# Performance work log

Hardware: AMD Instinct MI355X
Metric: run time of the kernel (lower is better)

Reference implementation:

```python
import jax, jax.numpy as jnp
import numpy as np

DIM, HEADS, MLP_RATIO = 384, 6, 4.0
HEAD_DIM = DIM // HEADS
HID = int(DIM * MLP_RATIO)
EPS = 1e-5


def _layer_norm(x, g, b):
    m = jnp.mean(x, axis=-1, keepdims=True)
    v = jnp.mean(jnp.square(x - m), axis=-1, keepdims=True)
    return (x - m) * jax.lax.rsqrt(v + EPS) * g + b


def setup_inputs() -> dict:
    key = jax.random.key(0)
    ks = jax.random.split(key, 16)
    B, N, C = 4, 2048, DIM
    s = 0.02
    return {
        "x": jax.random.normal(ks[0], (B, N, C), dtype=jnp.float32),
        "ln1_g": jnp.ones((C,), jnp.float32),
        "ln1_b": jnp.zeros((C,), jnp.float32),
        "qkv_w": jax.random.normal(ks[1], (C, 3 * C), jnp.float32) * s,  # [in, out]
        "qkv_b": jnp.zeros((3 * C,), jnp.float32),
        "proj_w": jax.random.normal(ks[2], (C, C), jnp.float32) * s,
        "proj_b": jnp.zeros((C,), jnp.float32),
        "ln2_g": jnp.ones((C,), jnp.float32),
        "ln2_b": jnp.zeros((C,), jnp.float32),
        "fc1_w": jax.random.normal(ks[3], (C, HID), jnp.float32) * s,
        "fc1_b": jnp.zeros((HID,), jnp.float32),
        "fc2_w": jax.random.normal(ks[4], (HID, C), jnp.float32) * s,
        "fc2_b": jnp.zeros((C,), jnp.float32),
    }


def reference(x, ln1_g, ln1_b, qkv_w, qkv_b, proj_w, proj_b,
              ln2_g, ln2_b, fc1_w, fc1_b, fc2_w, fc2_b):
    B, N, C = x.shape
    scale = HEAD_DIM ** (-0.5)

    # --- attention branch (pre-norm) ---
    h = _layer_norm(x, ln1_g, ln1_b)
    qkv = (h @ qkv_w + qkv_b).reshape(B, N, 3, HEADS, HEAD_DIM)
    qkv = jnp.transpose(qkv, (2, 0, 3, 1, 4))  # [3, B, H, N, D]
    q, k, v = qkv[0], qkv[1], qkv[2]
    attn = jnp.einsum("bhnd,bhmd->bhnm", q, k) * scale
    attn = jax.nn.softmax(attn, axis=-1)
    out = jnp.einsum("bhnm,bhmd->bhnd", attn, v)
    out = jnp.transpose(out, (0, 2, 1, 3)).reshape(B, N, C)
    x = x + (out @ proj_w + proj_b)

    # --- MLP branch (pre-norm) ---
    h = _layer_norm(x, ln2_g, ln2_b)
    h = jax.nn.gelu(h @ fc1_w + fc1_b, approximate=False)
    x = x + (h @ fc2_w + fc2_b)
    return x
```

## Files before the change

kernel.cpp:

```cpp
#include <hip/hip_runtime.h>

typedef unsigned short u16;
typedef unsigned int u32;
typedef __bf16 bf16x8_t __attribute__((ext_vector_type(8)));
typedef float f32x4 __attribute__((ext_vector_type(4)));
typedef float f32x16 __attribute__((ext_vector_type(16)));

__device__ __forceinline__ u16 f2b(float f) {
  union { float f; u32 u; } v; v.f = f;
  u32 r = v.u + 0x7fffu + ((v.u >> 16) & 1u);
  return (u16)(r >> 16);
}

__device__ __forceinline__ u32 pkbf(float a, float b) {
  union { __bf16 h[2]; u32 u; } v;
  v.h[0] = (__bf16)a; v.h[1] = (__bf16)b;
  return v.u;
}

__device__ __forceinline__ size_t fmoff(int r, int c, int Kd) {
  return ((size_t)(r >> 4) * (Kd >> 3) + (c >> 3)) * 128 + (r & 15) * 8 + (c & 7);
}

__device__ __forceinline__ f32x4 mfma16(uint4 a, uint4 b, f32x4 c) {
  return __builtin_amdgcn_mfma_f32_16x16x32_bf16(
      __builtin_bit_cast(bf16x8_t, a), __builtin_bit_cast(bf16x8_t, b), c, 0, 0, 0);
}

__device__ __forceinline__ f32x16 mfma32(uint4 a, uint4 b, f32x16 c) {
  return __builtin_amdgcn_mfma_f32_32x32x16_bf16(
      __builtin_bit_cast(bf16x8_t, a), __builtin_bit_cast(bf16x8_t, b), c, 0, 0, 0);
}

__device__ __forceinline__ void plswap(u32& a, u32& b) {
  asm("v_permlane32_swap_b32 %0, %1" : "+v"(a), "+v"(b));
}

__device__ __forceinline__ void load_lds16(const void* g, void* l) {
  __builtin_amdgcn_global_load_lds(
      (const __attribute__((address_space(1))) unsigned int*)g,
      (__attribute__((address_space(3))) unsigned int*)l, 16, 0, 0);
}

template <int N>
__device__ __forceinline__ void waitvm() {
  if constexpr (N == 0) asm volatile("s_waitcnt vmcnt(0)" ::: "memory");
  else if constexpr (N == 4) asm volatile("s_waitcnt vmcnt(4)" ::: "memory");
  else if constexpr (N == 6) asm volatile("s_waitcnt vmcnt(6)" ::: "memory");
  else if constexpr (N == 8) asm volatile("s_waitcnt vmcnt(8)" ::: "memory");
  else asm volatile("s_waitcnt vmcnt(10)" ::: "memory");
}

__device__ __forceinline__ void ln_body(const float* __restrict__ x,
                                        const float* __restrict__ g,
                                        const float* __restrict__ bta,
                                        u16* __restrict__ out, int row,
                                        int lane) {
  const float* xr = x + (size_t)row * 384;
  float v[6];
  float s = 0.f;
#pragma unroll
  for (int i = 0; i < 6; i++) { v[i] = xr[i * 64 + lane]; s += v[i]; }
#pragma unroll
  for (int off = 32; off >= 1; off >>= 1) s += __shfl_xor(s, off);
  float mean = s * (1.0f / 384.0f);
  float vs = 0.f;
#pragma unroll
  for (int i = 0; i < 6; i++) { float d = v[i] - mean; vs += d * d; }
#pragma unroll
  for (int off = 32; off >= 1; off >>= 1) vs += __shfl_xor(vs, off);
  float rstd = rsqrtf(vs * (1.0f / 384.0f) + 1e-5f);
#pragma unroll
  for (int i = 0; i < 6; i++) {
    int c = i * 64 + lane;
    out[fmoff(row, c, 384)] = f2b((v[i] - mean) * rstd * g[c] + bta[c]);
  }
}

__global__ __launch_bounds__(256) void ln_k(const float* __restrict__ x,
                                            const float* __restrict__ g,
                                            const float* __restrict__ bta,
                                            u16* __restrict__ out) {
  ln_body(x, g, bta, out, blockIdx.x * 4 + (threadIdx.x >> 6),
          threadIdx.x & 63);
}

__global__ __launch_bounds__(256) void prep_k(
    const float* __restrict__ w0, u16* __restrict__ t0_,
    const float* __restrict__ w1, u16* __restrict__ t1_,
    const float* __restrict__ w2, u16* __restrict__ t2_,
    const float* __restrict__ w3, u16* __restrict__ t3_,
    const float* __restrict__ x, const float* __restrict__ g,
    const float* __restrict__ bta, u16* __restrict__ lnout) {
  __shared__ u16 L[64][68];
  int tile = blockIdx.x, tid = threadIdx.x;
  if (tile >= 432) {
    ln_body(x, g, bta, lnout, (tile - 432) * 4 + (tid >> 6), tid & 63);
    return;
  }
  const float* w; u16* wt; int K, N, rel;
  if (tile < 108)      { w = w0; wt = t0_; K = 384;  N = 1152; rel = tile; }
  else if (tile < 144) { w = w1; wt = t1_; K = 384;  N = 384;  rel = tile - 108; }
  else if (tile < 288) { w = w2; wt = t2_; K = 384;  N = 1536; rel = tile - 144; }
  else                 { w = w3; wt = t3_; K = 1536; N = 384;  rel = tile - 288; }
  int ntx = N >> 6;
  int tk = (rel / ntx) << 6, tn = (rel - (rel / ntx) * ntx) << 6;

  int r = tid >> 2, c0 = (tid & 3) << 4;
  const float* src = w + (size_t)(tk + r) * N + tn + c0;
#pragma unroll
  for (int j = 0; j < 16; j += 4) {
    float4 a = *(const float4*)(src + j);
    L[r][c0 + j + 0] = f2b(a.x);
    L[r][c0 + j + 1] = f2b(a.y);
    L[r][c0 + j + 2] = f2b(a.z);
    L[r][c0 + j + 3] = f2b(a.w);
  }
  __syncthreads();
  int n = tid >> 2, k0 = (tid & 3) << 4;
  u16 tmp[16];
#pragma unroll
  for (int j = 0; j < 16; j++) tmp[j] = L[k0 + j][n];
  u16* dst = wt + (size_t)(tn + n) * K + tk + k0;
  *(uint4*)dst = *(const uint4*)(tmp);
  *(uint4*)(dst + 8) = *(const uint4*)(tmp + 8);
}

template <int EPI, int MR, int KD>
__global__ __launch_bounds__(256, 2) void gemm_k(
    const u16* __restrict__ A, const u16* __restrict__ Bt,
    const float* __restrict__ bias, const float* __restrict__ res,
    void* __restrict__ outp, int Nn,
    u16* __restrict__ qp, u16* __restrict__ kp, u16* __restrict__ vtp) {
  constexpr int NS = KD / 64;
  constexpr int KD8 = KD / 8;
  __shared__ __align__(16) u16 Bs[3][64 * 64];
  int tid = threadIdx.x;
  int lane = tid & 63, wid = tid >> 6;
  int li = lane & 15, lg = lane >> 4;
  int wr = wid >> 1, wc = wid & 1;
  int row0 = blockIdx.y * (MR * 32), col0 = blockIdx.x * 64;

  int lr = lane >> 3;
  int sc8 = ((lane & 7) ^ lr) * 8;

  const u16* Ab = A + ((size_t)(row0 / 16 + wr * MR) * KD8 + lg) * 128 + li * 8;

  f32x4 z = {0.f, 0.f, 0.f, 0.f};
  f32x4 acc[MR][2];
#pragma unroll
  for (int m = 0; m < MR; m++)
#pragma unroll
    for (int n = 0; n < 2; n++) acc[m][n] = z;

  uint4 af0[MR][2], af1[MR][2];

  auto stageB = [&](int buf, int k0) {
#pragma unroll
    for (int j = 0; j < 2; j++) {
      int ib = wid * 2 + j;
      load_lds16(Bt + (size_t)(col0 + ib * 8 + lr) * KD + k0 + sc8,
                 (char*)Bs[buf] + ib * 1024);
    }
  };
  auto loadA = [&](uint4 (*dst)[2], int t) {
#pragma unroll
    for (int m = 0; m < MR; m++)
#pragma unroll
      for (int kk = 0; kk < 2; kk++)
        dst[m][kk] =
            *(const uint4*)(Ab + ((size_t)m * KD8 + t * 8 + kk * 4) * 128);
  };

  stageB(0, 0);
  stageB(1, 64);
  loadA(af0, 0);
  if (NS > 1) loadA(af1, 1);
  waitvm<2 * MR>();
  __builtin_amdgcn_s_barrier();
  asm volatile("" ::: "memory");

#pragma unroll
  for (int t = 0; t < NS; t++) {
    if (t + 2 < NS) stageB((t + 2) % 3, (t + 2) * 64);
    const char* Bsb = (const char*)Bs[t % 3];
#pragma unroll
    for (int kk = 0; kk < 2; kk++) {
      uint4 bf[2];
#pragma unroll
      for (int n = 0; n < 2; n++) {
        int c = wc * 32 + n * 16 + li;
        bf[n] = *(const uint4*)(Bsb + c * 128 +
                                ((kk * 64 + lg * 16) ^ ((c & 7) << 4)));
      }
#pragma unroll
      for (int m = 0; m < MR; m++)
#pragma unroll
        for (int n = 0; n < 2; n++)
          acc[m][n] = mfma16((t & 1) ? af1[m][kk] : af0[m][kk], bf[n],
                             acc[m][n]);
    }
    if (t + 2 < NS) {
      if (t & 1) loadA(af1, t + 2);
      else       loadA(af0, t + 2);
      waitvm<2 + 2 * MR>();
      __builtin_amdgcn_s_barrier();
      asm volatile("" ::: "memory");
    } else if (t + 1 < NS) {
      waitvm<0>();
      __builtin_amdgcn_s_barrier();
      asm volatile("" ::: "memory");
    }
  }

#pragma unroll
  for (int m = 0; m < MR; m++) {
#pragma unroll
    for (int n = 0; n < 2; n++) {
#pragma unroll
      for (int j = 0; j < 4; j++) {
        int r = row0 + wr * (MR * 16) + m * 16 + lg * 4 + j;
        int c = col0 + wc * 32 + n * 16 + li;
        float v = acc[m][n][j] + bias[c];
        if (EPI == 0) {
          ((float*)outp)[(size_t)r * Nn + c] = v + res[(size_t)r * Nn + c];
        } else if (EPI == 1) {
          float e = __expf(-1.5957691f * v * (1.f + 0.044715f * v * v));
          ((u16*)outp)[fmoff(r, c, Nn)] = f2b(v / (1.f + e));
        } else {
          int tt = c / 384;
          int c2 = c - tt * 384;
          int hh = c2 >> 6, d = c2 & 63;
          int bb = r >> 11, nn = r & 2047;
          size_t bh = (size_t)bb * 6 + hh;
          int tile = nn >> 5;
          if (tt == 2) {
            int kvl = nn & 31;
            int kvHalf = (kvl >> 4) & 1, h2 = (kvl >> 3) & 1, jj = kvl & 7;
            int dTile = d >> 5, l31 = d & 31;
            vtp[(((bh * 64 + tile) * 2 + dTile) * 2 + kvHalf) * 512 +
                (l31 + h2 * 32) * 8 + jj] = f2b(v);
          } else {
            int chunk = d >> 4, h2 = (d >> 3) & 1, e = d & 7;
            int l31 = nn & 31;
            size_t off = ((bh * 64 + tile) * 4 + chunk) * 512 +
                         (l31 + h2 * 32) * 8 + e;
            if (tt == 0) qp[off] = f2b(v * 0.18033688f);
            else         kp[off] = f2b(v);
          }
        }
      }
    }
  }
}

__global__ __launch_bounds__(256, 3) void attn_k(const u16* __restrict__ q,
                                                 const u16* __restrict__ k,
                                                 const u16* __restrict__ vt,
                                                 u16* __restrict__ out) {
  __shared__ __align__(16) float Ol[3][2][16][64];
  __shared__ float Ls[3][64];

  int tid = threadIdx.x;
  int lane = tid & 63, wid = tid >> 6;
  int l31 = lane & 31, hi = lane >> 5;
  int bid = blockIdx.x;
  int nid = (bid & 7) * 192 + (bid >> 3);
  int bh = nid >> 6, qT = nid & 63;
  int b = bh / 6, hh = bh - b * 6;
  int qb = qT * 32;

  const u16* qp_ = q + ((size_t)bh * 64 + qT) * 2048 + lane * 8;
  const u16* kp_ = k + ((size_t)bh * 64 + wid * 16) * 2048 + lane * 8;
  const u16* vp_ = vt + ((size_t)bh * 64 + wid * 16) * 2048 + lane * 8;

  uint4 qf[4], kf[4];
#pragma unroll
  for (int c = 0; c < 4; c++) qf[c] = *(const uint4*)(qp_ + c * 512);
#pragma unroll
  for (int c = 0; c < 4; c++) kf[c] = *(const uint4*)(kp_ + c * 512);
  kp_ += 2048;

  f32x16 o0, o1;
#pragma unroll
  for (int r = 0; r < 16; r++) { o0[r] = 0.f; o1[r] = 0.f; }
  float lsum = 0.f;

#pragma unroll
  for (int t = 0; t < 16; t++) {
    uint4 vf0 = *(const uint4*)(vp_);
    uint4 vf1 = *(const uint4*)(vp_ + 512);
    uint4 vf2 = *(const uint4*)(vp_ + 1024);
    uint4 vf3 = *(const uint4*)(vp_ + 1536);
    uint4 kn[4];
    if (t < 15) {
#pragma unroll
      for (int c = 0; c < 4; c++) kn[c] = *(const uint4*)(kp_ + c * 512);
    }

    f32x16 s;
#pragma unroll
    for (int r = 0; r < 16; r++) s[r] = 0.f;
#pragma unroll
    for (int c = 0; c < 4; c++) s = mfma32(kf[c], qf[c], s);

    float p[16];
#pragma unroll
    for (int r = 0; r < 16; r++) p[r] = __builtin_amdgcn_exp2f(s[r]);
    lsum += ((p[0] + p[1]) + (p[2] + p[3])) + ((p[4] + p[5]) + (p[6] + p[7])) +
            ((p[8] + p[9]) + (p[10] + p[11])) +
            ((p[12] + p[13]) + (p[14] + p[15]));

    u32 u[8];
#pragma unroll
    for (int i = 0; i < 8; i++) u[i] = pkbf(p[2 * i], p[2 * i + 1]);
    plswap(u[0], u[2]); plswap(u[1], u[3]);
    plswap(u[4], u[6]); plswap(u[5], u[7]);
    uint4 pa0 = {u[0], u[1], u[2], u[3]};
    uint4 pa1 = {u[4], u[5], u[6], u[7]};

    o0 = mfma32(pa0, vf0, o0);
    o0 = mfma32(pa1, vf1, o0);
    o1 = mfma32(pa0, vf2, o1);
    o1 = mfma32(pa1, vf3, o1);

    if (t < 15) {
#pragma unroll
      for (int c = 0; c < 4; c++) kf[c] = kn[c];
    }
    kp_ += 2048;
    vp_ += 2048;
  }

  lsum += __shfl_xor(lsum, 32);

  if (wid) {
#pragma unroll
    for (int r = 0; r < 16; r++) {
      Ol[wid - 1][0][r][lane] = o0[r];
      Ol[wid - 1][1][r][lane] = o1[r];
    }
    Ls[wid - 1][lane] = lsum;
  }
  __syncthreads();
  if (wid == 0) {
#pragma unroll
    for (int w = 0; w < 3; w++) lsum += Ls[w][lane];
#pragma unroll
    for (int r = 0; r < 16; r++)
#pragma unroll
      for (int w = 0; w < 3; w++) {
        o0[r] += Ol[w][0][r][lane];
        o1[r] += Ol[w][1][r][lane];
      }
    float rl = 1.0f / lsum;
#pragma unroll
    for (int r = 0; r < 16; r++) {
      int qo = (r & 3) + 8 * (r >> 2) + hi * 4;
      float rlq = __shfl(rl, qo, 64);
      int row = b * 2048 + qb + qo;
      out[fmoff(row, hh * 64 + l31, 384)] = f2b(o0[r] * rlq);
      out[fmoff(row, hh * 64 + 32 + l31, 384)] = f2b(o1[r] * rlq);
    }
  }
}

extern "C" void kernel_launch(void* const* d_in, const int* in_sizes, int n_in,
                              void* d_out, int out_size, void* d_ws,
                              size_t ws_size, hipStream_t stream) {
  const float* x      = (const float*)d_in[0];
  const float* ln1_g  = (const float*)d_in[1];
  const float* ln1_b  = (const float*)d_in[2];
  const float* qkv_w  = (const float*)d_in[3];
  const float* qkv_b  = (const float*)d_in[4];
  const float* proj_w = (const float*)d_in[5];
  const float* proj_b = (const float*)d_in[6];
  const float* ln2_g  = (const float*)d_in[7];
  const float* ln2_b  = (const float*)d_in[8];
  const float* fc1_w  = (const float*)d_in[9];
  const float* fc1_b  = (const float*)d_in[10];
  const float* fc2_w  = (const float*)d_in[11];
  const float* fc2_b  = (const float*)d_in[12];
  float* out = (float*)d_out;

  char* p = (char*)d_ws;
  u16* qkvwt  = (u16*)p;  p += (size_t)1152 * 384 * 2;
  u16* projwt = (u16*)p;  p += (size_t)384 * 384 * 2;
  u16* fc1wt  = (u16*)p;  p += (size_t)1536 * 384 * 2;
  u16* fc2wt  = (u16*)p;  p += (size_t)384 * 1536 * 2;
  float* x1   = (float*)p; p += (size_t)8192 * 384 * 4;
  u16* reg1   = (u16*)p;  p += (size_t)8192 * 384 * 2;
  u16* reg2   = (u16*)p;  p += (size_t)8192 * 1536 * 2;
  u16* qd  = reg2;
  u16* kd  = reg2 + (size_t)24 * 2048 * 64;
  u16* vtd = kd + (size_t)24 * 2048 * 64;
  u16* h3  = reg2;

  prep_k<<<432 + 2048, 256, 0, stream>>>(qkv_w, qkvwt, proj_w, projwt,
                                         fc1_w, fc1wt, fc2_w, fc2wt,
                                         x, ln1_g, ln1_b, reg1);
  gemm_k<2, 4, 384><<<dim3(18, 64), 256, 0, stream>>>(
      reg1, qkvwt, qkv_b, nullptr, nullptr, 1152, qd, kd, vtd);
  attn_k<<<dim3(1536), 256, 0, stream>>>(qd, kd, vtd, reg1);
  gemm_k<0, 2, 384><<<dim3(6, 128), 256, 0, stream>>>(
      reg1, projwt, proj_b, x, x1, 384, nullptr, nullptr, nullptr);
  ln_k<<<2048, 256, 0, stream>>>(x1, ln2_g, ln2_b, reg1);
  gemm_k<1, 4, 384><<<dim3(24, 64), 256, 0, stream>>>(
      reg1, fc1wt, fc1_b, nullptr, h3, 1536, nullptr, nullptr, nullptr);
  gemm_k<0, 2, 1536><<<dim3(6, 128), 256, 0, stream>>>(
      h3, fc2wt, fc2_b, x1, out, 384, nullptr, nullptr, nullptr);
}
```

Measured before the change: 135.7 us.

## Swizzle GEMM block order, prefetch V in attention, split reduction across waves

GEMM launches become 1D grids with a swizzle that groups 8 row tiles per column tile for L2 reuse, and MR=2 GEMMs get a higher occupancy launch bound. In attention, V fragments are prefetched one iteration ahead alongside K, MFMA sections get raised wave priority, and the final cross-wave reduction is spread over all four waves instead of wave 0 alone. These target memory latency and the serialized epilogue, at the cost of extra registers and LDS that may reduce occupancy.

```diff
diff --git a/kernel.cpp b/kernel.cpp
--- a/kernel.cpp
+++ b/kernel.cpp
@@ -126,8 +126,8 @@
   *(uint4*)(dst + 8) = *(const uint4*)(tmp + 8);
 }
 
-template <int EPI, int MR, int KD>
-__global__ __launch_bounds__(256, 2) void gemm_k(
+template <int EPI, int MR, int KD, int NX, int MINW>
+__global__ __launch_bounds__(256, MINW) void gemm_k(
     const u16* __restrict__ A, const u16* __restrict__ Bt,
     const float* __restrict__ bias, const float* __restrict__ res,
     void* __restrict__ outp, int Nn,
@@ -139,7 +139,12 @@
   int lane = tid & 63, wid = tid >> 6;
   int li = lane & 15, lg = lane >> 4;
   int wr = wid >> 1, wc = wid & 1;
-  int row0 = blockIdx.y * (MR * 32), col0 = blockIdx.x * 64;
+
+  int p = blockIdx.x;
+  int idx = p >> 3;
+  int cx = idx % NX;
+  int row0 = ((p & 7) + ((idx / NX) << 3)) * (MR * 32);
+  int col0 = cx * 64;
 
   int lr = lane >> 3;
   int sc8 = ((lane & 7) ^ lr) * 8;
@@ -258,8 +263,8 @@
                                                  const u16* __restrict__ k,
                                                  const u16* __restrict__ vt,
                                                  u16* __restrict__ out) {
-  __shared__ __align__(16) float Ol[3][2][16][64];
-  __shared__ float Ls[3][64];
+  __shared__ __align__(16) float Ol[4][2][16][64];
+  __shared__ float Ls[4][64];
 
   int tid = threadIdx.x;
   int lane = tid & 63, wid = tid >> 6;
@@ -274,12 +279,15 @@
   const u16* kp_ = k + ((size_t)bh * 64 + wid * 16) * 2048 + lane * 8;
   const u16* vp_ = vt + ((size_t)bh * 64 + wid * 16) * 2048 + lane * 8;
 
-  uint4 qf[4], kf[4];
+  uint4 qf[4], kf[4], vf[4];
 #pragma unroll
   for (int c = 0; c < 4; c++) qf[c] = *(const uint4*)(qp_ + c * 512);
 #pragma unroll
   for (int c = 0; c < 4; c++) kf[c] = *(const uint4*)(kp_ + c * 512);
+#pragma unroll
+  for (int c = 0; c < 4; c++) vf[c] = *(const uint4*)(vp_ + c * 512);
   kp_ += 2048;
+  vp_ += 2048;
 
   f32x16 o0, o1;
 #pragma unroll
@@ -288,21 +296,21 @@
 
 #pragma unroll
   for (int t = 0; t < 16; t++) {
-    uint4 vf0 = *(const uint4*)(vp_);
-    uint4 vf1 = *(const uint4*)(vp_ + 512);
-    uint4 vf2 = *(const uint4*)(vp_ + 1024);
-    uint4 vf3 = *(const uint4*)(vp_ + 1536);
-    uint4 kn[4];
+    uint4 kn[4], vn[4];
     if (t < 15) {
 #pragma unroll
       for (int c = 0; c < 4; c++) kn[c] = *(const uint4*)(kp_ + c * 512);
+#pragma unroll
+      for (int c = 0; c < 4; c++) vn[c] = *(const uint4*)(vp_ + c * 512);
     }
 
     f32x16 s;
 #pragma unroll
     for (int r = 0; r < 16; r++) s[r] = 0.f;
+    __builtin_amdgcn_s_setprio(1);
 #pragma unroll
     for (int c = 0; c < 4; c++) s = mfma32(kf[c], qf[c], s);
+    __builtin_amdgcn_s_setprio(0);
 
     float p[16];
 #pragma unroll
@@ -319,14 +327,16 @@
     uint4 pa0 = {u[0], u[1], u[2], u[3]};
     uint4 pa1 = {u[4], u[5], u[6], u[7]};
 
-    o0 = mfma32(pa0, vf0, o0);
-    o0 = mfma32(pa1, vf1, o0);
-    o1 = mfma32(pa0, vf2, o1);
-    o1 = mfma32(pa1, vf3, o1);
+    __builtin_amdgcn_s_setprio(1);
+    o0 = mfma32(pa0, vf[0], o0);
+    o0 = mfma32(pa1, vf[1], o0);
+    o1 = mfma32(pa0, vf[2], o1);
+    o1 = mfma32(pa1, vf[3], o1);
+    __builtin_amdgcn_s_setprio(0);
 
     if (t < 15) {
 #pragma unroll
-      for (int c = 0; c < 4; c++) kf[c] = kn[c];
+      for (int c = 0; c < 4; c++) { kf[c] = kn[c]; vf[c] = vn[c]; }
     }
     kp_ += 2048;
     vp_ += 2048;
@@ -334,34 +344,27 @@
 
   lsum += __shfl_xor(lsum, 32);
 
-  if (wid) {
-#pragma unroll
-    for (int r = 0; r < 16; r++) {
-      Ol[wid - 1][0][r][lane] = o0[r];
-      Ol[wid - 1][1][r][lane] = o1[r];
-    }
-    Ls[wid - 1][lane] = lsum;
-  }
+#pragma unroll
+  for (int r = 0; r < 16; r++) {
+    Ol[wid][0][r][lane] = o0[r];
+    Ol[wid][1][r][lane] = o1[r];
+  }
+  Ls[wid][lane] = lsum;
   __syncthreads();
-  if (wid == 0) {
-#pragma unroll
-    for (int w = 0; w < 3; w++) lsum += Ls[w][lane];
-#pragma unroll
-    for (int r = 0; r < 16; r++)
-#pragma unroll
-      for (int w = 0; w < 3; w++) {
-        o0[r] += Ol[w][0][r][lane];
-        o1[r] += Ol[w][1][r][lane];
-      }
-    float rl = 1.0f / lsum;
-#pragma unroll
-    for (int r = 0; r < 16; r++) {
-      int qo = (r & 3) + 8 * (r >> 2) + hi * 4;
-      float rlq = __shfl(rl, qo, 64);
-      int row = b * 2048 + qb + qo;
-      out[fmoff(row, hh * 64 + l31, 384)] = f2b(o0[r] * rlq);
-      out[fmoff(row, hh * 64 + 32 + l31, 384)] = f2b(o1[r] * rlq);
-    }
+  float lt = (Ls[0][lane] + Ls[1][lane]) + (Ls[2][lane] + Ls[3][lane]);
+  float rl = 1.0f / lt;
+#pragma unroll
+  for (int rr = 0; rr < 4; rr++) {
+    int r = wid * 4 + rr;
+    float s0 = (Ol[0][0][r][lane] + Ol[1][0][r][lane]) +
+               (Ol[2][0][r][lane] + Ol[3][0][r][lane]);
+    float s1 = (Ol[0][1][r][lane] + Ol[1][1][r][lane]) +
+               (Ol[2][1][r][lane] + Ol[3][1][r][lane]);
+    int qo = (r & 3) + 8 * (r >> 2) + hi * 4;
+    float rlq = __shfl(rl, qo, 64);
+    int row = b * 2048 + qb + qo;
+    out[fmoff(row, hh * 64 + l31, 384)] = f2b(s0 * rlq);
+    out[fmoff(row, hh * 64 + 32 + l31, 384)] = f2b(s1 * rlq);
   }
 }
 
@@ -399,14 +402,14 @@
   prep_k<<<432 + 2048, 256, 0, stream>>>(qkv_w, qkvwt, proj_w, projwt,
                                          fc1_w, fc1wt, fc2_w, fc2wt,
                                          x, ln1_g, ln1_b, reg1);
-  gemm_k<2, 4, 384><<<dim3(18, 64), 256, 0, stream>>>(
+  gemm_k<2, 4, 384, 18, 2><<<dim3(1152), 256, 0, stream>>>(
       reg1, qkvwt, qkv_b, nullptr, nullptr, 1152, qd, kd, vtd);
   attn_k<<<dim3(1536), 256, 0, stream>>>(qd, kd, vtd, reg1);
-  gemm_k<0, 2, 384><<<dim3(6, 128), 256, 0, stream>>>(
+  gemm_k<0, 2, 384, 6, 4><<<dim3(768), 256, 0, stream>>>(
       reg1, projwt, proj_b, x, x1, 384, nullptr, nullptr, nullptr);
   ln_k<<<2048, 256, 0, stream>>>(x1, ln2_g, ln2_b, reg1);
-  gemm_k<1, 4, 384><<<dim3(24, 64), 256, 0, stream>>>(
+  gemm_k<1, 4, 384, 24, 2><<<dim3(1536), 256, 0, stream>>>(
       reg1, fc1wt, fc1_b, nullptr, h3, 1536, nullptr, nullptr, nullptr);
-  gemm_k<0, 2, 1536><<<dim3(6, 128), 256, 0, stream>>>(
+  gemm_k<0, 2, 1536, 6, 4><<<dim3(768), 256, 0, stream>>>(
       h3, fc2wt, fc2_b, x1, out, 384, nullptr, nullptr, nullptr);
 }
```

New measurement: 141.9 us. 1.05x slower.
